# Kernel tuning notes

Hardware: AMD Instinct MI355X
Metric: run time of the kernel (lower is better)

## Reference

```python
import jax, jax.numpy as jnp
import numpy as np

N_NODES = 50000
N_EDGES = 1600000
IN_DIM = 1024
HID = 128
N_GRAPHS = 64


def setup_inputs() -> dict:
    key = jax.random.key(0)
    ks = jax.random.split(key, 8)
    x = jax.random.normal(ks[0], (N_NODES, IN_DIM), dtype=jnp.float32)
    edge_index = jax.random.randint(ks[1], (2, N_EDGES), 0, N_NODES, dtype=jnp.int32)
    batch = jnp.sort(jax.random.randint(ks[2], (N_NODES,), 0, N_GRAPHS, dtype=jnp.int32))
    # GATConv parameters (single head, concat irrelevant for 1 head)
    glorot = 1.0 / np.sqrt(IN_DIM)
    W = jax.random.uniform(ks[3], (IN_DIM, HID), minval=-glorot, maxval=glorot, dtype=jnp.float32)
    ga = 1.0 / np.sqrt(HID)
    att_src = jax.random.uniform(ks[4], (HID,), minval=-ga, maxval=ga, dtype=jnp.float32)
    att_dst = jax.random.uniform(ks[5], (HID,), minval=-ga, maxval=ga, dtype=jnp.float32)
    bias = jnp.zeros((HID,), dtype=jnp.float32)
    return {"x": x, "W": W, "att_src": att_src, "att_dst": att_dst, "bias": bias,
            "edge_index": edge_index, "batch": batch, "num_graphs": N_GRAPHS}


def reference(x, W, att_src, att_dst, bias, edge_index, batch, num_graphs):
    N = x.shape[0]
    h = x @ W                               # [N, HID]
    # add self-loops (GATConv default add_self_loops=True)
    loops = jnp.arange(N, dtype=edge_index.dtype)
    src = jnp.concatenate([edge_index[0], loops])   # [E+N]
    dst = jnp.concatenate([edge_index[1], loops])
    a_src = h @ att_src                     # [N]
    a_dst = h @ att_dst                     # [N]
    e = jax.nn.leaky_relu(a_src[src] + a_dst[dst], negative_slope=0.2)  # [E+N]
    # scatter-softmax over incoming edges of each destination node
    m = jax.ops.segment_max(e, dst, num_segments=N)
    p = jnp.exp(e - m[dst])
    denom = jax.ops.segment_sum(p, dst, num_segments=N)
    alpha = p / denom[dst]                  # [E+N]
    # attention-weighted aggregation
    out = jax.ops.segment_sum(alpha[:, None] * h[src], dst, num_segments=N)  # [N, HID]
    out = jax.nn.relu(out + bias)
    # global max pool over graphs in the batch
    return jax.ops.segment_max(out, batch, num_segments=num_graphs)          # [G, HID]
```

## Files before the change

### kernel.cpp

```cpp
#include <hip/hip_runtime.h>
#include <hip/hip_bf16.h>

#define N_NODES 50000
#define N_EDGES 1600000
#define IN_DIM 1024
#define HID 128
#define AGG_WAVES 6144

typedef __bf16 bf16x8 __attribute__((ext_vector_type(8)));
typedef float f32x4 __attribute__((ext_vector_type(4)));
typedef __bf16 bf16x4 __attribute__((ext_vector_type(4)));

__device__ __forceinline__ float2 bf2f(unsigned u) {
    return make_float2(__uint_as_float(u << 16), __uint_as_float(u & 0xffff0000u));
}
__device__ __forceinline__ float lrelu(float v) { return v > 0.f ? v : 0.2f * v; }

__global__ void prep_kernel(const float* __restrict__ W, __bf16* __restrict__ wt,
                            int* __restrict__ deg, float* __restrict__ out, int out_n) {
    int i = blockIdx.x * 256 + threadIdx.x;
    if (i < N_NODES) deg[i] = 0;
    if (i < out_n) out[i] = 0.0f;
    if (i < HID * IN_DIM) {
        int n = i >> 10, k = i & 1023;
        wt[i] = (__bf16)W[(size_t)k * HID + n];
    }
}

__global__ __launch_bounds__(256) void gemm_kernel(const float* __restrict__ x,
                                                   const __bf16* __restrict__ wt,
                                                   __bf16* __restrict__ h2,
                                                   const float* __restrict__ att_s,
                                                   const float* __restrict__ att_d,
                                                   float* __restrict__ o_as,
                                                   float* __restrict__ o_ad) {
    __shared__ __bf16 xa[2][64][40];
    __shared__ __bf16 wb[2][128][40];
    const int t = threadIdx.x;
    const int m0 = blockIdx.x * 64;
    const int wid = t >> 6, lane = t & 63;
    const int lm = lane & 15, q8 = (lane >> 4) * 8;
    const int rw0 = wid * 16;

    float4 xs_reg[2];
    uint2  ws_reg[4];

    auto stage_regs = [&](int k0) {
#pragma unroll
        for (int l = 0; l < 2; ++l) {
            int f = t + l * 256;
            int row = f >> 3, kq = f & 7;
            int gr = m0 + row;
            float4 v = make_float4(0.f, 0.f, 0.f, 0.f);
            if (gr < N_NODES)
                v = *(const float4*)(x + (size_t)gr * IN_DIM + k0 + kq * 4);
            xs_reg[l] = v;
        }
#pragma unroll
        for (int l = 0; l < 4; ++l) {
            int f = t + l * 256;
            int n = f >> 3, c = f & 7;
            ws_reg[l] = *(const uint2*)(wt + (size_t)n * IN_DIM + k0 + c * 4);
        }
    };
    auto regs_to_lds = [&](int b) {
#pragma unroll
        for (int l = 0; l < 2; ++l) {
            int f = t + l * 256;
            int row = f >> 3, kq = f & 7;
            bf16x4 v;
            v[0] = (__bf16)xs_reg[l].x; v[1] = (__bf16)xs_reg[l].y;
            v[2] = (__bf16)xs_reg[l].z; v[3] = (__bf16)xs_reg[l].w;
            *(bf16x4*)&xa[b][row][kq * 4] = v;
        }
#pragma unroll
        for (int l = 0; l < 4; ++l) {
            int f = t + l * 256;
            int n = f >> 3, c = f & 7;
            *(uint2*)&wb[b][n][c * 4] = ws_reg[l];
        }
    };

    f32x4 acc[8] = {};
    stage_regs(0);
    regs_to_lds(0);
    __syncthreads();
    for (int it = 0; it < 32; ++it) {
        const int cur = it & 1;
        if (it + 1 < 32) stage_regs((it + 1) * 32);
        bf16x8 af = *(const bf16x8*)&xa[cur][rw0 + lm][q8];
#pragma unroll
        for (int ct = 0; ct < 8; ++ct) {
            bf16x8 bfr = *(const bf16x8*)&wb[cur][ct * 16 + lm][q8];
            acc[ct] = __builtin_amdgcn_mfma_f32_16x16x32_bf16(af, bfr, acc[ct], 0, 0, 0);
        }
        if (it + 1 < 32) {
            regs_to_lds(cur ^ 1);
            __syncthreads();
        }
    }
    const int quad = lane >> 4;
    float attsf[8], attdf[8];
#pragma unroll
    for (int ct = 0; ct < 8; ++ct) {
        attsf[ct] = att_s[ct * 16 + lm];
        attdf[ct] = att_d[ct * 16 + lm];
    }
#pragma unroll
    for (int reg = 0; reg < 4; ++reg) {
        int row = m0 + rw0 + quad * 4 + reg;
        float ps = 0.f, pd = 0.f;
#pragma unroll
        for (int ct = 0; ct < 8; ++ct) {
            float v = acc[ct][reg];
            ps = fmaf(v, attsf[ct], ps);
            pd = fmaf(v, attdf[ct], pd);
        }
#pragma unroll
        for (int o = 8; o; o >>= 1) {
            ps += __shfl_xor(ps, o);
            pd += __shfl_xor(pd, o);
        }
        if (row < N_NODES) {
            if (lm == 0) { o_as[row] = ps; o_ad[row] = pd; }
#pragma unroll
            for (int ct = 0; ct < 8; ++ct)
                h2[(size_t)row * HID + ct * 16 + lm] = (__bf16)acc[ct][reg];
        }
    }
}

__global__ void hist_kernel(const int* __restrict__ ei, int* __restrict__ deg,
                            int* __restrict__ epos) {
    int e = blockIdx.x * 256 + threadIdx.x;
    if (e < N_EDGES) epos[e] = atomicAdd(&deg[ei[N_EDGES + e]], 1);
}

__global__ void scan1_kernel(const int* __restrict__ deg, int* __restrict__ bsum) {
    int b = blockIdx.x, t = threadIdx.x;
    int base = b * 1024 + t * 4;
    int s = 0;
#pragma unroll
    for (int j = 0; j < 4; ++j) {
        int idx = base + j;
        if (idx < N_NODES) s += deg[idx];
    }
    for (int o = 32; o; o >>= 1) s += __shfl_xor(s, o);
    __shared__ int wsum[4];
    int lane = t & 63, w = t >> 6;
    if (lane == 0) wsum[w] = s;
    __syncthreads();
    if (t == 0) bsum[b] = wsum[0] + wsum[1] + wsum[2] + wsum[3];
}

__global__ void scan2_kernel(const int* __restrict__ bsum, int* __restrict__ boff,
                             int* __restrict__ rowstart, int nb) {
    if (threadIdx.x == 0 && blockIdx.x == 0) {
        int run = 0;
        for (int i = 0; i < nb; ++i) { boff[i] = run; run += bsum[i]; }
        rowstart[N_NODES] = run;
    }
}

__global__ void scan3_kernel(const int* __restrict__ deg, const int* __restrict__ boff,
                             int* __restrict__ rowstart) {
    int b = blockIdx.x, t = threadIdx.x;
    int base = b * 1024 + t * 4;
    int v[4]; int s = 0;
#pragma unroll
    for (int j = 0; j < 4; ++j) {
        int idx = base + j;
        v[j] = (idx < N_NODES) ? deg[idx] : 0;
        s += v[j];
    }
    int lane = t & 63, w = t >> 6;
    int inc = s;
    for (int o = 1; o < 64; o <<= 1) {
        int u = __shfl_up(inc, o);
        if (lane >= o) inc += u;
    }
    __shared__ int wt[4];
    if (lane == 63) wt[w] = inc;
    __syncthreads();
    int woff = 0;
    for (int i = 0; i < w; ++i) woff += wt[i];
    int run = woff + inc - s + boff[b];
#pragma unroll
    for (int j = 0; j < 4; ++j) {
        int idx = base + j;
        if (idx < N_NODES) {
            rowstart[idx] = run;
            run += v[j];
        }
    }
}

__global__ void scatter_kernel(const int* __restrict__ ei, const int* __restrict__ rowstart,
                               const int* __restrict__ epos, uint2* __restrict__ csrp,
                               const float* __restrict__ a_src) {
    int e = blockIdx.x * 256 + threadIdx.x;
    if (e >= N_EDGES) return;
    int s = ei[e], d = ei[N_EDGES + e];
    uint2 v; v.x = (unsigned)s; v.y = __float_as_uint(a_src[s]);
    csrp[rowstart[d] + epos[e]] = v;
}

__global__ __launch_bounds__(256, 6) void aggregate_kernel(
    const unsigned* __restrict__ h2u, const float* __restrict__ a_src,
    const float* __restrict__ a_dst, const int* __restrict__ rowstart,
    const uint2* __restrict__ csrp, const float* __restrict__ bias,
    const int* __restrict__ batch, float* __restrict__ out) {
    const int wid = threadIdx.x >> 6, lane = threadIdx.x & 63;
    const int w = blockIdx.x * 4 + wid;
    const int q = N_NODES / AGG_WAVES;
    const int r = N_NODES - q * AGG_WAVES;
    int n0 = w * q + (w < r ? w : r);
    int n1 = n0 + q + (w < r ? 1 : 0);
    const float b0 = bias[2 * lane], b1 = bias[2 * lane + 1];

    int gcur = -1;
    float m0 = 0.f, m1 = 0.f;
    for (int n = n0; n < n1; ++n) {
        int rs = rowstart[n], re = rowstart[n + 1];
        float adn = a_dst[n];
        float pself = __expf(lrelu(a_src[n] + adn));
        float2 hv = bf2f(h2u[(size_t)n * 64 + lane]);
        float denom = pself;
        float2 acc = make_float2(pself * hv.x, pself * hv.y);
        for (int base = rs; base < re; base += 64) {
            int cnt = re - base; if (cnt > 64) cnt = 64;
            uint2 sp = make_uint2(0u, 0u);
            bool valid = (base + lane < re);
            if (valid) sp = csrp[base + lane];
            float pe = valid ? __expf(lrelu(__uint_as_float(sp.y) + adn)) : 0.f;
            float ds = pe;
            for (int o = 32; o; o >>= 1) ds += __shfl_xor(ds, o);
            denom += ds;
            for (int e = 0; e < cnt; e += 16) {
                unsigned uu[16]; float pp[16];
#pragma unroll
                for (int i = 0; i < 16; ++i) {
                    unsigned src = (unsigned)__shfl((int)sp.x, e + i);
                    pp[i] = __shfl(pe, e + i);
                    uu[i] = h2u[(size_t)src * 64 + lane];
                }
#pragma unroll
                for (int i = 0; i < 16; ++i) {
                    float2 g = bf2f(uu[i]);
                    acc.x = fmaf(pp[i], g.x, acc.x);
                    acc.y = fmaf(pp[i], g.y, acc.y);
                }
            }
        }
        float inv = 1.0f / denom;
        float o0 = fmaxf(acc.x * inv + b0, 0.0f);
        float o1 = fmaxf(acc.y * inv + b1, 0.0f);
        int g = batch[n];
        if (g != gcur) {
            if (gcur >= 0) {
                unsigned* outp = (unsigned*)(out + (size_t)gcur * HID);
                atomicMax(&outp[2 * lane], __float_as_uint(m0));
                atomicMax(&outp[2 * lane + 1], __float_as_uint(m1));
            }
            gcur = g; m0 = o0; m1 = o1;
        } else {
            m0 = fmaxf(m0, o0); m1 = fmaxf(m1, o1);
        }
    }
    if (gcur >= 0) {
        unsigned* outp = (unsigned*)(out + (size_t)gcur * HID);
        atomicMax(&outp[2 * lane], __float_as_uint(m0));
        atomicMax(&outp[2 * lane + 1], __float_as_uint(m1));
    }
}

extern "C" void kernel_launch(void* const* d_in, const int* in_sizes, int n_in,
                              void* d_out, int out_size, void* d_ws, size_t ws_size,
                              hipStream_t stream) {
    const float* x     = (const float*)d_in[0];
    const float* W     = (const float*)d_in[1];
    const float* att_s = (const float*)d_in[2];
    const float* att_d = (const float*)d_in[3];
    const float* bias  = (const float*)d_in[4];
    const int*   ei    = (const int*)d_in[5];
    const int*   batch = (const int*)d_in[6];
    float*       out   = (float*)d_out;

    char* ws = (char*)d_ws;
    size_t off = 0;
    auto alloc = [&](size_t bytes) -> void* {
        void* p = ws + off;
        off += (bytes + 255) & ~(size_t)255;
        return p;
    };
    const int NB = (N_NODES + 1023) / 1024;
    __bf16* h2       = (__bf16*)alloc((size_t)N_NODES * HID * 2);
    __bf16* wt       = (__bf16*)alloc((size_t)HID * IN_DIM * 2);
    float*  a_src    = (float*)alloc((size_t)N_NODES * 4);
    float*  a_dst    = (float*)alloc((size_t)N_NODES * 4);
    int*    deg      = (int*)alloc((size_t)N_NODES * 4);
    int*    rowstart = (int*)alloc((size_t)(N_NODES + 1) * 4);
    int*    bsum     = (int*)alloc((size_t)NB * 4);
    int*    boff     = (int*)alloc((size_t)NB * 4);
    int*    epos     = (int*)alloc((size_t)N_EDGES * 4);
    uint2*  csrp     = (uint2*)alloc((size_t)N_EDGES * 8);
    (void)ws_size; (void)in_sizes; (void)n_in;

    hipLaunchKernelGGL(prep_kernel, dim3(512), dim3(256), 0, stream,
                       W, wt, deg, out, out_size);
    hipLaunchKernelGGL(gemm_kernel, dim3((N_NODES + 63) / 64), dim3(256), 0, stream,
                       x, wt, h2, att_s, att_d, a_src, a_dst);
    hipLaunchKernelGGL(hist_kernel, dim3((N_EDGES + 255) / 256), dim3(256), 0, stream,
                       ei, deg, epos);
    hipLaunchKernelGGL(scan1_kernel, dim3(NB), dim3(256), 0, stream, deg, bsum);
    hipLaunchKernelGGL(scan2_kernel, dim3(1), dim3(64), 0, stream, bsum, boff, rowstart, NB);
    hipLaunchKernelGGL(scan3_kernel, dim3(NB), dim3(256), 0, stream, deg, boff, rowstart);
    hipLaunchKernelGGL(scatter_kernel, dim3((N_EDGES + 255) / 256), dim3(256), 0, stream,
                       ei, rowstart, epos, csrp, a_src);
    hipLaunchKernelGGL(aggregate_kernel, dim3(AGG_WAVES / 4), dim3(256), 0, stream,
                       (const unsigned*)h2, a_src, a_dst, rowstart, csrp, bias, batch, out);
}
```

Measured before the change: 507.5 us.

## Precompute edge attention weights in scatter and gather neighbor rows with 16-byte loads

Edge attention weights exp(lrelu(a_src+a_dst)) are now computed once in the scatter kernel, and self-loop weights in the GEMM epilogue. The per-edge position array is dropped in favour of an atomic cursor per destination. The aggregate kernel splits the wave into four 16-lane quads, each loading a full 256-byte neighbor row with uint4 loads, so four edges are processed per load instruction. Partial sums are then reduced across quads. Softmax max-subtraction remains skipped as before, and the atomic cursor makes edge order within a row nondeterministic.

```diff
diff --git a/kernel.cpp b/kernel.cpp
--- a/kernel.cpp
+++ b/kernel.cpp
@@ -33,7 +33,8 @@
                                                    const float* __restrict__ att_s,
                                                    const float* __restrict__ att_d,
                                                    float* __restrict__ o_as,
-                                                   float* __restrict__ o_ad) {
+                                                   float* __restrict__ o_ad,
+                                                   float* __restrict__ o_ps) {
     __shared__ __bf16 xa[2][64][40];
     __shared__ __bf16 wb[2][128][40];
     const int t = threadIdx.x;
@@ -122,7 +123,10 @@
             pd += __shfl_xor(pd, o);
         }
         if (row < N_NODES) {
-            if (lm == 0) { o_as[row] = ps; o_ad[row] = pd; }
+            if (lm == 0) {
+                o_as[row] = ps; o_ad[row] = pd;
+                o_ps[row] = __expf(lrelu(ps + pd));
+            }
 #pragma unroll
             for (int ct = 0; ct < 8; ++ct)
                 h2[(size_t)row * HID + ct * 16 + lm] = (__bf16)acc[ct][reg];
@@ -130,10 +134,9 @@
     }
 }
 
-__global__ void hist_kernel(const int* __restrict__ ei, int* __restrict__ deg,
-                            int* __restrict__ epos) {
+__global__ void hist_kernel(const int* __restrict__ ei, int* __restrict__ deg) {
     int e = blockIdx.x * 256 + threadIdx.x;
-    if (e < N_EDGES) epos[e] = atomicAdd(&deg[ei[N_EDGES + e]], 1);
+    if (e < N_EDGES) atomicAdd(&deg[ei[N_EDGES + e]], 1);
 }
 
 __global__ void scan1_kernel(const int* __restrict__ deg, int* __restrict__ bsum) {
@@ -163,7 +166,7 @@
 }
 
 __global__ void scan3_kernel(const int* __restrict__ deg, const int* __restrict__ boff,
-                             int* __restrict__ rowstart) {
+                             int* __restrict__ rowstart, int* __restrict__ cursor) {
     int b = blockIdx.x, t = threadIdx.x;
     int base = b * 1024 + t * 4;
     int v[4]; int s = 0;
@@ -190,87 +193,118 @@
         int idx = base + j;
         if (idx < N_NODES) {
             rowstart[idx] = run;
+            cursor[idx] = run;
             run += v[j];
         }
     }
 }
 
-__global__ void scatter_kernel(const int* __restrict__ ei, const int* __restrict__ rowstart,
-                               const int* __restrict__ epos, uint2* __restrict__ csrp,
-                               const float* __restrict__ a_src) {
+__global__ void scatter_kernel(const int* __restrict__ ei, int* __restrict__ cursor,
+                               uint2* __restrict__ csrp, const float* __restrict__ a_src,
+                               const float* __restrict__ a_dst) {
     int e = blockIdx.x * 256 + threadIdx.x;
     if (e >= N_EDGES) return;
     int s = ei[e], d = ei[N_EDGES + e];
-    uint2 v; v.x = (unsigned)s; v.y = __float_as_uint(a_src[s]);
-    csrp[rowstart[d] + epos[e]] = v;
+    int slot = atomicAdd(&cursor[d], 1);
+    float pe = __expf(lrelu(a_src[s] + a_dst[d]));
+    uint2 v; v.x = (unsigned)s; v.y = __float_as_uint(pe);
+    csrp[slot] = v;
 }
 
 __global__ __launch_bounds__(256, 6) void aggregate_kernel(
-    const unsigned* __restrict__ h2u, const float* __restrict__ a_src,
-    const float* __restrict__ a_dst, const int* __restrict__ rowstart,
-    const uint2* __restrict__ csrp, const float* __restrict__ bias,
-    const int* __restrict__ batch, float* __restrict__ out) {
+    const uint4* __restrict__ h2q, const float* __restrict__ pself_a,
+    const int* __restrict__ rowstart, const uint2* __restrict__ csrp,
+    const float* __restrict__ bias, const int* __restrict__ batch,
+    float* __restrict__ out) {
     const int wid = threadIdx.x >> 6, lane = threadIdx.x & 63;
     const int w = blockIdx.x * 4 + wid;
+    const int quad = lane >> 4, ql = lane & 15;
+    const int vq = quad << 2;
     const int q = N_NODES / AGG_WAVES;
     const int r = N_NODES - q * AGG_WAVES;
     int n0 = w * q + (w < r ? w : r);
     int n1 = n0 + q + (w < r ? 1 : 0);
-    const float b0 = bias[2 * lane], b1 = bias[2 * lane + 1];
+
+    float bl[8];
+    {
+        const float4* b4 = (const float4*)bias;
+        float4 x0 = b4[ql * 2], x1 = b4[ql * 2 + 1];
+        bl[0] = x0.x; bl[1] = x0.y; bl[2] = x0.z; bl[3] = x0.w;
+        bl[4] = x1.x; bl[5] = x1.y; bl[6] = x1.z; bl[7] = x1.w;
+    }
 
     int gcur = -1;
     float m0 = 0.f, m1 = 0.f;
     for (int n = n0; n < n1; ++n) {
         int rs = rowstart[n], re = rowstart[n + 1];
-        float adn = a_dst[n];
-        float pself = __expf(lrelu(a_src[n] + adn));
-        float2 hv = bf2f(h2u[(size_t)n * 64 + lane]);
-        float denom = pself;
-        float2 acc = make_float2(pself * hv.x, pself * hv.y);
+        float psf = pself_a[n];
+        uint4 sv = h2q[(size_t)n * 16 + ql];
+        float w0 = (quad == 0) ? psf : 0.f;
+        float a[8];
+        {
+            float2 f0 = bf2f(sv.x), f1 = bf2f(sv.y), f2 = bf2f(sv.z), f3 = bf2f(sv.w);
+            a[0] = w0 * f0.x; a[1] = w0 * f0.y; a[2] = w0 * f1.x; a[3] = w0 * f1.y;
+            a[4] = w0 * f2.x; a[5] = w0 * f2.y; a[6] = w0 * f3.x; a[7] = w0 * f3.y;
+        }
+        float pws = 0.f;
         for (int base = rs; base < re; base += 64) {
             int cnt = re - base; if (cnt > 64) cnt = 64;
             uint2 sp = make_uint2(0u, 0u);
-            bool valid = (base + lane < re);
-            if (valid) sp = csrp[base + lane];
-            float pe = valid ? __expf(lrelu(__uint_as_float(sp.y) + adn)) : 0.f;
-            float ds = pe;
-            for (int o = 32; o; o >>= 1) ds += __shfl_xor(ds, o);
-            denom += ds;
-            for (int e = 0; e < cnt; e += 16) {
-                unsigned uu[16]; float pp[16];
-#pragma unroll
-                for (int i = 0; i < 16; ++i) {
-                    unsigned src = (unsigned)__shfl((int)sp.x, e + i);
-                    pp[i] = __shfl(pe, e + i);
-                    uu[i] = h2u[(size_t)src * 64 + lane];
+            if (base + lane < re) sp = csrp[base + lane];
+            int ngrp = (cnt + 3) >> 2;
+            ngrp = (ngrp + 3) & ~3;
+            for (int g = 0; g < ngrp; g += 4) {
+                uint4 uu[4]; float pw[4];
+#pragma unroll
+                for (int i = 0; i < 4; ++i) {
+                    int bidx = ((g + i) << 4) + vq;
+                    unsigned bs = (unsigned)__builtin_amdgcn_ds_bpermute(bidx, (int)sp.x);
+                    unsigned bp = (unsigned)__builtin_amdgcn_ds_bpermute(bidx, (int)sp.y);
+                    pw[i] = __uint_as_float(bp);
+                    uu[i] = h2q[bs * 16u + (unsigned)ql];
                 }
 #pragma unroll
-                for (int i = 0; i < 16; ++i) {
-                    float2 g = bf2f(uu[i]);
-                    acc.x = fmaf(pp[i], g.x, acc.x);
-                    acc.y = fmaf(pp[i], g.y, acc.y);
+                for (int i = 0; i < 4; ++i) {
+                    float2 f0 = bf2f(uu[i].x), f1 = bf2f(uu[i].y);
+                    float2 f2 = bf2f(uu[i].z), f3 = bf2f(uu[i].w);
+                    float p = pw[i];
+                    a[0] = fmaf(p, f0.x, a[0]); a[1] = fmaf(p, f0.y, a[1]);
+                    a[2] = fmaf(p, f1.x, a[2]); a[3] = fmaf(p, f1.y, a[3]);
+                    a[4] = fmaf(p, f2.x, a[4]); a[5] = fmaf(p, f2.y, a[5]);
+                    a[6] = fmaf(p, f3.x, a[6]); a[7] = fmaf(p, f3.y, a[7]);
+                    pws += p;
                 }
             }
         }
-        float inv = 1.0f / denom;
-        float o0 = fmaxf(acc.x * inv + b0, 0.0f);
-        float o1 = fmaxf(acc.y * inv + b1, 0.0f);
+#pragma unroll
+        for (int k = 0; k < 8; ++k) {
+            a[k] += __shfl_xor(a[k], 16);
+            a[k] += __shfl_xor(a[k], 32);
+        }
+        pws += __shfl_xor(pws, 16);
+        pws += __shfl_xor(pws, 32);
+        float inv = 1.0f / (psf + pws);
+        float o[8];
+#pragma unroll
+        for (int k = 0; k < 8; ++k) o[k] = fmaxf(fmaf(a[k], inv, bl[k]), 0.f);
+        float s0 = quad == 0 ? o[0] : quad == 1 ? o[2] : quad == 2 ? o[4] : o[6];
+        float s1 = quad == 0 ? o[1] : quad == 1 ? o[3] : quad == 2 ? o[5] : o[7];
         int g = batch[n];
         if (g != gcur) {
             if (gcur >= 0) {
                 unsigned* outp = (unsigned*)(out + (size_t)gcur * HID);
-                atomicMax(&outp[2 * lane], __float_as_uint(m0));
-                atomicMax(&outp[2 * lane + 1], __float_as_uint(m1));
+                atomicMax(&outp[ql * 8 + 2 * quad],     __float_as_uint(m0));
+                atomicMax(&outp[ql * 8 + 2 * quad + 1], __float_as_uint(m1));
             }
-            gcur = g; m0 = o0; m1 = o1;
+            gcur = g; m0 = s0; m1 = s1;
         } else {
-            m0 = fmaxf(m0, o0); m1 = fmaxf(m1, o1);
+            m0 = fmaxf(m0, s0); m1 = fmaxf(m1, s1);
         }
     }
     if (gcur >= 0) {
         unsigned* outp = (unsigned*)(out + (size_t)gcur * HID);
-        atomicMax(&outp[2 * lane], __float_as_uint(m0));
-        atomicMax(&outp[2 * lane + 1], __float_as_uint(m1));
+        atomicMax(&outp[ql * 8 + 2 * quad],     __float_as_uint(m0));
+        atomicMax(&outp[ql * 8 + 2 * quad + 1], __float_as_uint(m1));
     }
 }
 
@@ -298,25 +332,26 @@
     __bf16* wt       = (__bf16*)alloc((size_t)HID * IN_DIM * 2);
     float*  a_src    = (float*)alloc((size_t)N_NODES * 4);
     float*  a_dst    = (float*)alloc((size_t)N_NODES * 4);
+    float*  pself    = (float*)alloc((size_t)N_NODES * 4);
     int*    deg      = (int*)alloc((size_t)N_NODES * 4);
     int*    rowstart = (int*)alloc((size_t)(N_NODES + 1) * 4);
+    int*    cursor   = (int*)alloc((size_t)N_NODES * 4);
     int*    bsum     = (int*)alloc((size_t)NB * 4);
     int*    boff     = (int*)alloc((size_t)NB * 4);
-    int*    epos     = (int*)alloc((size_t)N_EDGES * 4);
     uint2*  csrp     = (uint2*)alloc((size_t)N_EDGES * 8);
     (void)ws_size; (void)in_sizes; (void)n_in;
 
     hipLaunchKernelGGL(prep_kernel, dim3(512), dim3(256), 0, stream,
                        W, wt, deg, out, out_size);
     hipLaunchKernelGGL(gemm_kernel, dim3((N_NODES + 63) / 64), dim3(256), 0, stream,
-                       x, wt, h2, att_s, att_d, a_src, a_dst);
+                       x, wt, h2, att_s, att_d, a_src, a_dst, pself);
     hipLaunchKernelGGL(hist_kernel, dim3((N_EDGES + 255) / 256), dim3(256), 0, stream,
-                       ei, deg, epos);
+                       ei, deg);
     hipLaunchKernelGGL(scan1_kernel, dim3(NB), dim3(256), 0, stream, deg, bsum);
     hipLaunchKernelGGL(scan2_kernel, dim3(1), dim3(64), 0, stream, bsum, boff, rowstart, NB);
-    hipLaunchKernelGGL(scan3_kernel, dim3(NB), dim3(256), 0, stream, deg, boff, rowstart);
+    hipLaunchKernelGGL(scan3_kernel, dim3(NB), dim3(256), 0, stream, deg, boff, rowstart, cursor);
     hipLaunchKernelGGL(scatter_kernel, dim3((N_EDGES + 255) / 256), dim3(256), 0, stream,
-                       ei, rowstart, epos, csrp, a_src);
+                       ei, cursor, csrp, a_src, a_dst);
     hipLaunchKernelGGL(aggregate_kernel, dim3(AGG_WAVES / 4), dim3(256), 0, stream,
-                       (const unsigned*)h2, a_src, a_dst, rowstart, csrp, bias, batch, out);
-}
+                       (const uint4*)h2, pself, rowstart, csrp, bias, batch, out);
+}
```

Result: slower. 522.4 us (+2.9%).

## Precompute edge attention weights as fp16 packed with source index in CSR

Applied to the files above, without the earlier changes.

Edge attention weights exp(leaky_relu(a_src+a_dst)) are now computed once in the scatter pass and stored as fp16 in the upper half of a 32-bit CSR entry, with the source index in the lower 16 bits. This halves the CSR footprint and removes the exp work from the aggregation loop. The per-edge epos array is dropped in favour of an atomic cursor per destination, and self-loop weights come precomputed from the GEMM epilogue. Aggregation also gets more waves and higher occupancy. Risks include fp16 precision loss on the weights, which are not max-shifted, and a 16-bit index limit that truncates node ids above 65535. N_NODES is 50000, so the indices still fit.

```diff
diff --git a/kernel.cpp b/kernel.cpp
--- a/kernel.cpp
+++ b/kernel.cpp
@@ -5,7 +5,7 @@
 #define N_EDGES 1600000
 #define IN_DIM 1024
 #define HID 128
-#define AGG_WAVES 6144
+#define AGG_WAVES 8192
 
 typedef __bf16 bf16x8 __attribute__((ext_vector_type(8)));
 typedef float f32x4 __attribute__((ext_vector_type(4)));
@@ -15,6 +15,9 @@
     return make_float2(__uint_as_float(u << 16), __uint_as_float(u & 0xffff0000u));
 }
 __device__ __forceinline__ float lrelu(float v) { return v > 0.f ? v : 0.2f * v; }
+__device__ __forceinline__ float f16tof(unsigned bits) {
+    return (float)__builtin_bit_cast(_Float16, (unsigned short)bits);
+}
 
 __global__ void prep_kernel(const float* __restrict__ W, __bf16* __restrict__ wt,
                             int* __restrict__ deg, float* __restrict__ out, int out_n) {
@@ -33,7 +36,8 @@
                                                    const float* __restrict__ att_s,
                                                    const float* __restrict__ att_d,
                                                    float* __restrict__ o_as,
-                                                   float* __restrict__ o_ad) {
+                                                   float* __restrict__ o_ad,
+                                                   float* __restrict__ o_ps) {
     __shared__ __bf16 xa[2][64][40];
     __shared__ __bf16 wb[2][128][40];
     const int t = threadIdx.x;
@@ -122,7 +126,10 @@
             pd += __shfl_xor(pd, o);
         }
         if (row < N_NODES) {
-            if (lm == 0) { o_as[row] = ps; o_ad[row] = pd; }
+            if (lm == 0) {
+                o_as[row] = ps; o_ad[row] = pd;
+                o_ps[row] = __expf(lrelu(ps + pd));
+            }
 #pragma unroll
             for (int ct = 0; ct < 8; ++ct)
                 h2[(size_t)row * HID + ct * 16 + lm] = (__bf16)acc[ct][reg];
@@ -130,10 +137,9 @@
     }
 }
 
-__global__ void hist_kernel(const int* __restrict__ ei, int* __restrict__ deg,
-                            int* __restrict__ epos) {
+__global__ void hist_kernel(const int* __restrict__ ei, int* __restrict__ deg) {
     int e = blockIdx.x * 256 + threadIdx.x;
-    if (e < N_EDGES) epos[e] = atomicAdd(&deg[ei[N_EDGES + e]], 1);
+    if (e < N_EDGES) atomicAdd(&deg[ei[N_EDGES + e]], 1);
 }
 
 __global__ void scan1_kernel(const int* __restrict__ deg, int* __restrict__ bsum) {
@@ -163,7 +169,7 @@
 }
 
 __global__ void scan3_kernel(const int* __restrict__ deg, const int* __restrict__ boff,
-                             int* __restrict__ rowstart) {
+                             int* __restrict__ rowstart, int* __restrict__ cursor) {
     int b = blockIdx.x, t = threadIdx.x;
     int base = b * 1024 + t * 4;
     int v[4]; int s = 0;
@@ -190,26 +196,29 @@
         int idx = base + j;
         if (idx < N_NODES) {
             rowstart[idx] = run;
+            cursor[idx] = run;
             run += v[j];
         }
     }
 }
 
-__global__ void scatter_kernel(const int* __restrict__ ei, const int* __restrict__ rowstart,
-                               const int* __restrict__ epos, uint2* __restrict__ csrp,
-                               const float* __restrict__ a_src) {
+__global__ void scatter_kernel(const int* __restrict__ ei, int* __restrict__ cursor,
+                               unsigned* __restrict__ csrp, const float* __restrict__ a_src,
+                               const float* __restrict__ a_dst) {
     int e = blockIdx.x * 256 + threadIdx.x;
     if (e >= N_EDGES) return;
     int s = ei[e], d = ei[N_EDGES + e];
-    uint2 v; v.x = (unsigned)s; v.y = __float_as_uint(a_src[s]);
-    csrp[rowstart[d] + epos[e]] = v;
-}
-
-__global__ __launch_bounds__(256, 6) void aggregate_kernel(
-    const unsigned* __restrict__ h2u, const float* __restrict__ a_src,
-    const float* __restrict__ a_dst, const int* __restrict__ rowstart,
-    const uint2* __restrict__ csrp, const float* __restrict__ bias,
-    const int* __restrict__ batch, float* __restrict__ out) {
+    int slot = atomicAdd(&cursor[d], 1);
+    float pe = __expf(lrelu(a_src[s] + a_dst[d]));
+    unsigned short hb = __builtin_bit_cast(unsigned short, (_Float16)pe);
+    csrp[slot] = (unsigned)s | ((unsigned)hb << 16);
+}
+
+__global__ __launch_bounds__(256, 8) void aggregate_kernel(
+    const unsigned* __restrict__ h2u, const float* __restrict__ pself_a,
+    const int* __restrict__ rowstart, const unsigned* __restrict__ csrp,
+    const float* __restrict__ bias, const int* __restrict__ batch,
+    float* __restrict__ out) {
     const int wid = threadIdx.x >> 6, lane = threadIdx.x & 63;
     const int w = blockIdx.x * 4 + wid;
     const int q = N_NODES / AGG_WAVES;
@@ -222,39 +231,36 @@
     float m0 = 0.f, m1 = 0.f;
     for (int n = n0; n < n1; ++n) {
         int rs = rowstart[n], re = rowstart[n + 1];
-        float adn = a_dst[n];
-        float pself = __expf(lrelu(a_src[n] + adn));
-        float2 hv = bf2f(h2u[(size_t)n * 64 + lane]);
-        float denom = pself;
-        float2 acc = make_float2(pself * hv.x, pself * hv.y);
+        float psf = pself_a[n];
+        float2 hv = bf2f(h2u[((unsigned)n << 6) | (unsigned)lane]);
+        float denom = psf;
+        float2 acc = make_float2(psf * hv.x, psf * hv.y);
         for (int base = rs; base < re; base += 64) {
             int cnt = re - base; if (cnt > 64) cnt = 64;
-            uint2 sp = make_uint2(0u, 0u);
-            bool valid = (base + lane < re);
-            if (valid) sp = csrp[base + lane];
-            float pe = valid ? __expf(lrelu(__uint_as_float(sp.y) + adn)) : 0.f;
-            float ds = pe;
+            unsigned sp = 0u;
+            if (base + lane < re) sp = csrp[base + lane];
+            float ds = f16tof(sp >> 16);
             for (int o = 32; o; o >>= 1) ds += __shfl_xor(ds, o);
             denom += ds;
             for (int e = 0; e < cnt; e += 16) {
-                unsigned uu[16]; float pp[16];
+                unsigned bb[16], uu[16];
 #pragma unroll
                 for (int i = 0; i < 16; ++i) {
-                    unsigned src = (unsigned)__shfl((int)sp.x, e + i);
-                    pp[i] = __shfl(pe, e + i);
-                    uu[i] = h2u[(size_t)src * 64 + lane];
+                    bb[i] = (unsigned)__shfl((int)sp, e + i);
+                    uu[i] = h2u[((bb[i] & 0xffffu) << 6) | (unsigned)lane];
                 }
 #pragma unroll
                 for (int i = 0; i < 16; ++i) {
                     float2 g = bf2f(uu[i]);
-                    acc.x = fmaf(pp[i], g.x, acc.x);
-                    acc.y = fmaf(pp[i], g.y, acc.y);
+                    float p = f16tof(bb[i] >> 16);
+                    acc.x = fmaf(p, g.x, acc.x);
+                    acc.y = fmaf(p, g.y, acc.y);
                 }
             }
         }
         float inv = 1.0f / denom;
-        float o0 = fmaxf(acc.x * inv + b0, 0.0f);
-        float o1 = fmaxf(acc.y * inv + b1, 0.0f);
+        float o0 = fmaxf(fmaf(acc.x, inv, b0), 0.0f);
+        float o1 = fmaxf(fmaf(acc.y, inv, b1), 0.0f);
         int g = batch[n];
         if (g != gcur) {
             if (gcur >= 0) {
@@ -294,29 +300,30 @@
         return p;
     };
     const int NB = (N_NODES + 1023) / 1024;
-    __bf16* h2       = (__bf16*)alloc((size_t)N_NODES * HID * 2);
-    __bf16* wt       = (__bf16*)alloc((size_t)HID * IN_DIM * 2);
-    float*  a_src    = (float*)alloc((size_t)N_NODES * 4);
-    float*  a_dst    = (float*)alloc((size_t)N_NODES * 4);
-    int*    deg      = (int*)alloc((size_t)N_NODES * 4);
-    int*    rowstart = (int*)alloc((size_t)(N_NODES + 1) * 4);
-    int*    bsum     = (int*)alloc((size_t)NB * 4);
-    int*    boff     = (int*)alloc((size_t)NB * 4);
-    int*    epos     = (int*)alloc((size_t)N_EDGES * 4);
-    uint2*  csrp     = (uint2*)alloc((size_t)N_EDGES * 8);
+    __bf16*   h2       = (__bf16*)alloc((size_t)N_NODES * HID * 2);
+    __bf16*   wt       = (__bf16*)alloc((size_t)HID * IN_DIM * 2);
+    float*    a_src    = (float*)alloc((size_t)N_NODES * 4);
+    float*    a_dst    = (float*)alloc((size_t)N_NODES * 4);
+    float*    pself    = (float*)alloc((size_t)N_NODES * 4);
+    int*      deg      = (int*)alloc((size_t)N_NODES * 4);
+    int*      rowstart = (int*)alloc((size_t)(N_NODES + 1) * 4);
+    int*      cursor   = (int*)alloc((size_t)N_NODES * 4);
+    int*      bsum     = (int*)alloc((size_t)NB * 4);
+    int*      boff     = (int*)alloc((size_t)NB * 4);
+    unsigned* csrp     = (unsigned*)alloc((size_t)N_EDGES * 4);
     (void)ws_size; (void)in_sizes; (void)n_in;
 
     hipLaunchKernelGGL(prep_kernel, dim3(512), dim3(256), 0, stream,
                        W, wt, deg, out, out_size);
     hipLaunchKernelGGL(gemm_kernel, dim3((N_NODES + 63) / 64), dim3(256), 0, stream,
-                       x, wt, h2, att_s, att_d, a_src, a_dst);
+                       x, wt, h2, att_s, att_d, a_src, a_dst, pself);
     hipLaunchKernelGGL(hist_kernel, dim3((N_EDGES + 255) / 256), dim3(256), 0, stream,
-                       ei, deg, epos);
+                       ei, deg);
     hipLaunchKernelGGL(scan1_kernel, dim3(NB), dim3(256), 0, stream, deg, bsum);
     hipLaunchKernelGGL(scan2_kernel, dim3(1), dim3(64), 0, stream, bsum, boff, rowstart, NB);
-    hipLaunchKernelGGL(scan3_kernel, dim3(NB), dim3(256), 0, stream, deg, boff, rowstart);
+    hipLaunchKernelGGL(scan3_kernel, dim3(NB), dim3(256), 0, stream, deg, boff, rowstart, cursor);
     hipLaunchKernelGGL(scatter_kernel, dim3((N_EDGES + 255) / 256), dim3(256), 0, stream,
-                       ei, rowstart, epos, csrp, a_src);
+                       ei, cursor, csrp, a_src, a_dst);
     hipLaunchKernelGGL(aggregate_kernel, dim3(AGG_WAVES / 4), dim3(256), 0, stream,
-                       (const unsigned*)h2, a_src, a_dst, rowstart, csrp, bias, batch, out);
-}
+                       (const unsigned*)h2, pself, rowstart, csrp, bias, batch, out);
+}
```

Result: slower. 583.2 us (+14.9%).
